# Kernel optimization log

Hardware: AMD Instinct MI355X
Metric: run time of the kernel (lower is better)

## Reference

```python
import jax, jax.numpy as jnp
from jax import lax
import numpy as np

TAU = 2.0      # LIF membrane time constant
VTH = 1.0      # spikingjelly LIFNode default v_threshold
ALPHA = 2.0    # spikingjelly surrogate.ATan default alpha

# Heaviside spike with ATan surrogate gradient (spikingjelly semantics)
@jax.custom_vjp
def spike(x):
    return (x >= 0.0).astype(x.dtype)

def _spike_fwd(x):
    return spike(x), x

def _spike_bwd(x, g):
    sg = (ALPHA / 2.0) / (1.0 + (jnp.pi / 2.0 * ALPHA * x) ** 2)
    return (g * sg,)

spike.defvjp(_spike_fwd, _spike_bwd)

def lif_step(v, x):
    # decay_input=True, v_reset=0.0, hard reset (spikingjelly LIFNode defaults)
    v = v + (x - v) / TAU
    s = spike(v - VTH)
    v = v * (1.0 - s)
    return v, s

def conv1d_same(x, k):
    # x: [N, L], k: [K]  -> depthwise-style 1D conv with SAME padding
    y = lax.conv_general_dilated(x[:, None, :], k[None, None, :], (1,), 'SAME')
    return y[:, 0, :]

def setup_inputs() -> dict:
    key = jax.random.key(0)
    ks = jax.random.split(key, 16)
    N, T, D, C, NC = 4096, 16, 700, 128, 20
    def lin(kw, kb, fout, fin):
        s = 1.0 / np.sqrt(fin)
        W = jax.random.uniform(kw, (fout, fin), jnp.float32, -s, s)
        b = jax.random.uniform(kb, (fout,), jnp.float32, -s, s)
        return W, b
    x = jax.random.normal(ks[0], (N, T, D), jnp.float32)
    W_in, b_in = lin(ks[1], ks[2], C, D)
    W_rec, b_rec = lin(ks[3], ks[4], C, C)
    W2, b2 = lin(ks[5], ks[6], C, C)
    k_t = jax.random.normal(ks[7], (3,), jnp.float32) * 0.5   # TATCA temporal conv, kernel_size_t=3
    k_c = jax.random.normal(ks[8], (3,), jnp.float32) * 0.5   # TATCA channel conv
    W_p, b_p = lin(ks[9], ks[10], C, C)
    W_out, b_out = lin(ks[11], ks[12], NC, C)
    return {"x": x, "W_in": W_in, "b_in": b_in, "W_rec": W_rec, "b_rec": b_rec,
            "W2": W2, "b2": b2, "k_t": k_t, "k_c": k_c,
            "W_p": W_p, "b_p": b_p, "W_out": W_out, "b_out": b_out}

def reference(x, W_in, b_in, W_rec, b_rec, W2, b2, k_t, k_c, W_p, b_p, W_out, b_out):
    N, T, D = x.shape
    C = W_in.shape[0]
    z = jnp.zeros((N, C), x.dtype)

    def step(carry, frame):
        v1, v2, spikes_last = carry
        inp = frame @ W_in.T + b_in + spikes_last @ W_rec.T + b_rec
        v1, s1 = lif_step(v1, inp)
        x2 = s1 @ W2.T + b2
        v2, feat = lif_step(v2, x2)
        return (v1, v2, s1), feat

    xs = jnp.transpose(x, (1, 0, 2))          # [T, N, D]
    _, features = lax.scan(step, (z, z, z), xs)  # [T, N, C]

    # TATCA_1D: temporal attention (conv over T, kernel 3) x channel attention (conv over C)
    t_att = jax.nn.sigmoid(conv1d_same(features.mean(2).T, k_t)).T   # [T, N]
    c_att = jax.nn.sigmoid(conv1d_same(features.mean(0), k_c))       # [N, C]
    attended = features * t_att[:, :, None] * c_att[None, :, :]

    def step2(v3, feat):
        h = feat @ W_p.T + b_p
        v3, s = lif_step(v3, h)
        return v3, s @ W_out.T + b_out

    _, outs = lax.scan(step2, z, attended)    # [T, N, num_classes]
    return outs.mean(0), features, attended
```

## Files before the change

kernel.cpp:

```cpp
#include <hip/hip_runtime.h>
#include <hip/hip_bf16.h>
#include <stdint.h>


typedef __attribute__((ext_vector_type(8))) _Float16 half8;
typedef __attribute__((ext_vector_type(4))) float f32x4;
typedef unsigned long long u64;

#define MFMA16F(a, b, c) __builtin_amdgcn_mfma_f32_16x16x32_f16(a, b, c, 0, 0, 0)

__device__ inline void gload16(const void* g, void* l) {
  __builtin_amdgcn_global_load_lds(
      (const __attribute__((address_space(1))) uint32_t*)g,
      (__attribute__((address_space(3))) uint32_t*)l, 16, 0, 0);
}

__device__ inline void splitf16(float4 q0, float4 q1, half8& hh, half8& ll) {
  float f[8] = {q0.x, q0.y, q0.z, q0.w, q1.x, q1.y, q1.z, q1.w};
  _Float16 H[8], L[8];
#pragma unroll
  for (int j = 0; j < 8; ++j) {
    _Float16 h1 = (_Float16)(f[j] * 16.0f);
    float r = fmaf((float)h1, -0.0625f, f[j]);
    L[j] = (_Float16)(r * 32768.0f);
    H[j] = h1;
  }
  __builtin_memcpy(&hh, H, 16);
  __builtin_memcpy(&ll, L, 16);
}

__global__ void k_prep(const float* __restrict__ Wr, const float* __restrict__ W2,
                       const float* __restrict__ Wp, const float* __restrict__ Win,
                       float* __restrict__ WrT, float* __restrict__ W2T,
                       float* __restrict__ WpT, ushort* __restrict__ F2) {
  int idx = blockIdx.x * blockDim.x + threadIdx.x;
  if (idx < 3 * 16384) {
    int sel = idx >> 14;
    int r = idx & 16383;
    int j = r >> 7, c = r & 127;
    const float* src = (sel == 0) ? Wr : (sel == 1) ? W2 : Wp;
    float* dst = (sel == 0) ? WrT : (sel == 1) ? W2T : WpT;
    dst[r] = src[c * 128 + j];
  } else {
    int i2 = idx - 49152;
    if (i2 >= 128 * 704) return;
    int c = i2 / 704, d = i2 - c * 704;
    float w = (d < 700) ? Win[c * 700 + d] : 0.f;
    _Float16 b1 = (_Float16)(w * 256.0f);
    float r = fmaf((float)b1, -0.00390625f, w);
    _Float16 b2 = (_Float16)(r * 524288.0f);
    ushort u1, u2;
    __builtin_memcpy(&u1, &b1, 2);
    __builtin_memcpy(&u2, &b2, 2);
    F2[i2] = u1;
    F2[90112 + i2] = u2;
  }
}

__global__ __launch_bounds__(256, 4) void k_gemm_scan(
    const float* __restrict__ x, const ushort* __restrict__ F2,
    const float* __restrict__ b_in, const float* __restrict__ b_rec,
    const float* __restrict__ WrT, const float* __restrict__ W2T,
    const float* __restrict__ b2, const float* __restrict__ WpT,
    const float* __restrict__ b_p, const float* __restrict__ W_out,
    const float* __restrict__ b_out, const float* __restrict__ k_t,
    const float* __restrict__ k_c, float* __restrict__ features,
    float* __restrict__ attended, float* __restrict__ out0) {
  __shared__ __align__(16) char lds[39424];

  const int tid = threadIdx.x;
  const int w = tid >> 6;
  const int l = tid & 63;
  const int blk = blockIdx.x;
  const int lm = l & 15, kh = l >> 4;

  const float* xr = x + (size_t)(blk * 64 + w * 16 + lm) * 700;

  const ushort* bsrc[4];
  int bdst[4];
#pragma unroll
  for (int i = 0; i < 4; ++i) {
    int idx = w * 4 + i;
    int plane = idx >> 3, cg = idx & 7;
    int col = cg * 16 + (l >> 2);
    bsrc[i] = F2 + plane * 90112 + col * 704 + (((l & 3) ^ ((l >> 3) & 3)) * 8);
    bdst[i] = plane * 8192 + cg * 1024;
  }
  const int bkey = (lm >> 1) & 3;
  const int brd = lm * 64 + ((kh ^ bkey) * 16);

  f32x4 acc_h[8], acc_m[8];
#pragma unroll
  for (int j = 0; j < 8; ++j) {
    acc_h[j] = (f32x4){0.f, 0.f, 0.f, 0.f};
    acc_m[j] = (f32x4){0.f, 0.f, 0.f, 0.f};
  }

  auto STAGE = [&](int buf, int kt) {
    const int k0 = kt * 32;
#pragma unroll
    for (int i = 0; i < 4; ++i)
      gload16(bsrc[i] + k0, lds + buf * 16384 + bdst[i]);
  };
  auto LOADA = [&](int kt, float4& q0, float4& q1) {
    const int k0 = kt * 32 + kh * 8;
    q0 = *(const float4*)(xr + k0);
    if (kt == 21 && kh == 3)
      q1 = make_float4(0.f, 0.f, 0.f, 0.f);
    else
      q1 = *(const float4*)(xr + k0 + 4);
  };

  STAGE(0, 0);
  float4 qa, qb;
  LOADA(0, qa, qb);
  __syncthreads();
  int buf = 0;
  for (int kt = 0; kt < 22; ++kt) {
    float4 na = {}, nb = {};
    if (kt < 21) {
      STAGE(buf ^ 1, kt + 1);
      LOADA(kt + 1, na, nb);
    }
    half8 a1, a2;
    splitf16(qa, qb, a1, a2);
    const char* bb0 = lds + buf * 16384 + brd;
#pragma unroll
    for (int nf = 0; nf < 8; ++nf) {
      const char* bb = bb0 + nf * 1024;
      half8 b1 = *(const half8*)(bb);
      half8 b2f = *(const half8*)(bb + 8192);
      acc_h[nf] = MFMA16F(a1, b1, acc_h[nf]);
      acc_m[nf] = MFMA16F(a1, b2f, acc_m[nf]);
      acc_m[nf] = MFMA16F(a2, b1, acc_m[nf]);
    }
    __syncthreads();
    qa = na; qb = nb;
    buf ^= 1;
  }

  float* XWs = (float*)lds;
#pragma unroll
  for (int nf = 0; nf < 8; ++nf) {
    const int col = nf * 16 + lm;
    const float bias = b_in[col] + b_rec[col];
    const int rowb = w * 16 + kh * 4;
#pragma unroll
    for (int r = 0; r < 4; ++r)
      XWs[(rowb + r) * 130 + col] =
          acc_h[nf][r] * 0.000244140625f +
          acc_m[nf][r] * 1.1920928955078125e-7f + bias;
  }

  const int n_glob = blk * 4 + w;
  char* sc = lds + 33280 + w * 1536;
  u64* fmaskp = (u64*)sc;
  float* tap = (float*)(sc + 256);
  float* cap = (float*)(sc + 320);
  float* gp = (float*)(sc + 832);

  const float b2a = b2[l], b2b = b2[l + 64];
  float v1a = 0.f, v1b = 0.f, v2a = 0.f, v2b = 0.f, fsa = 0.f, fsb = 0.f;
  u64 pm0 = 0ull, pm1 = 0ull;

  for (int t = 0; t < 16; ++t) {
    const float* xrow = XWs + (w * 16 + t) * 130;
    float ia = xrow[l];
    float ib = xrow[l + 64];
    u64 q0 = pm0, q1 = pm1;
    while (q0) { int j = __builtin_ctzll(q0); q0 &= q0 - 1;
      ia += WrT[j * 128 + l]; ib += WrT[j * 128 + l + 64]; }
    while (q1) { int j = __builtin_ctzll(q1); q1 &= q1 - 1;
      ia += WrT[(64 + j) * 128 + l]; ib += WrT[(64 + j) * 128 + l + 64]; }
    v1a = v1a + (ia - v1a) * 0.5f;
    bool sa = (v1a - 1.0f) >= 0.f; v1a = sa ? 0.f : v1a;
    v1b = v1b + (ib - v1b) * 0.5f;
    bool sb = (v1b - 1.0f) >= 0.f; v1b = sb ? 0.f : v1b;
    pm0 = __ballot((int)sa);
    pm1 = __ballot((int)sb);
    float xa = b2a, xb = b2b;
    u64 r0 = pm0, r1 = pm1;
    while (r0) { int j = __builtin_ctzll(r0); r0 &= r0 - 1;
      xa += W2T[j * 128 + l]; xb += W2T[j * 128 + l + 64]; }
    while (r1) { int j = __builtin_ctzll(r1); r1 &= r1 - 1;
      xa += W2T[(64 + j) * 128 + l]; xb += W2T[(64 + j) * 128 + l + 64]; }
    v2a = v2a + (xa - v2a) * 0.5f;
    bool fa = (v2a - 1.0f) >= 0.f; v2a = fa ? 0.f : v2a;
    v2b = v2b + (xb - v2b) * 0.5f;
    bool fb = (v2b - 1.0f) >= 0.f; v2b = fb ? 0.f : v2b;
    float ffa = fa ? 1.f : 0.f, ffb = fb ? 1.f : 0.f;
    features[(size_t)((t << 12) | n_glob) * 128 + l] = ffa;
    features[(size_t)((t << 12) | n_glob) * 128 + l + 64] = ffb;
    fsa += ffa; fsb += ffb;
    u64 f0 = __ballot((int)fa), f1 = __ballot((int)fb);
    if (l == 0) { fmaskp[t * 2 + 0] = f0; fmaskp[t * 2 + 1] = f1; }
  }

  gp[l] = fsa * (1.f / 16.f);
  gp[l + 64] = fsb * (1.f / 16.f);

  if (l < 16) {
    float acc = 0.f;
#pragma unroll
    for (int j = 0; j < 3; ++j) {
      int tt = l - 1 + j;
      if (tt >= 0 && tt < 16) {
        float m = (float)(__popcll(fmaskp[tt * 2 + 0]) +
                          __popcll(fmaskp[tt * 2 + 1])) * (1.f / 128.f);
        acc += k_t[j] * m;
      }
    }
    tap[l] = 1.f / (1.f + expf(-acc));
  }
  {
    float mm1 = (l == 0) ? 0.f : gp[l - 1];
    float acc = k_c[0] * mm1 + k_c[1] * gp[l] + k_c[2] * gp[l + 1];
    cap[l] = 1.f / (1.f + expf(-acc));
    float np1 = (l == 63) ? 0.f : gp[l + 65];
    float acc2 = k_c[0] * gp[l + 63] + k_c[1] * gp[l + 64] + k_c[2] * np1;
    cap[l + 64] = 1.f / (1.f + expf(-acc2));
  }

  const float bpa = b_p[l], bpb = b_p[l + 64];
  const float caa = cap[l], cab = cap[l + 64];
  float v3a = 0.f, v3b = 0.f, ssa = 0.f, ssb = 0.f;
  for (int t = 0; t < 16; ++t) {
    u64 m0 = fmaskp[t * 2 + 0], m1 = fmaskp[t * 2 + 1];
    float tat = tap[t];
    bool ba = (m0 >> l) & 1, bb = (m1 >> l) & 1;
    attended[(size_t)((t << 12) | n_glob) * 128 + l] = ba ? tat * caa : 0.f;
    attended[(size_t)((t << 12) | n_glob) * 128 + l + 64] = bb ? tat * cab : 0.f;
    float ha = bpa, hb = bpb;
    u64 q0 = m0, q1 = m1;
    while (q0) { int j = __builtin_ctzll(q0); q0 &= q0 - 1;
      float w_ = tat * cap[j];
      ha += w_ * WpT[j * 128 + l]; hb += w_ * WpT[j * 128 + l + 64]; }
    while (q1) { int j = __builtin_ctzll(q1); q1 &= q1 - 1;
      float w_ = tat * cap[64 + j];
      ha += w_ * WpT[(64 + j) * 128 + l]; hb += w_ * WpT[(64 + j) * 128 + l + 64]; }
    v3a = v3a + (ha - v3a) * 0.5f;
    bool sa = (v3a - 1.0f) >= 0.f; v3a = sa ? 0.f : v3a;
    ssa += sa ? 1.f : 0.f;
    v3b = v3b + (hb - v3b) * 0.5f;
    bool sb = (v3b - 1.0f) >= 0.f; v3b = sb ? 0.f : v3b;
    ssb += sb ? 1.f : 0.f;
  }
  gp[l] = ssa * (1.f / 16.f);
  gp[l + 64] = ssb * (1.f / 16.f);
  if (l < 20) {
    float acc = b_out[l];
    for (int j = 0; j < 128; ++j) acc += gp[j] * W_out[l * 128 + j];
    out0[n_glob * 20 + l] = acc;
  }
}

extern "C" void kernel_launch(void* const* d_in, const int* in_sizes, int n_in,
                              void* d_out, int out_size, void* d_ws, size_t ws_size,
                              hipStream_t stream) {
  const float* x     = (const float*)d_in[0];
  const float* W_in  = (const float*)d_in[1];
  const float* b_in  = (const float*)d_in[2];
  const float* W_rec = (const float*)d_in[3];
  const float* b_rec = (const float*)d_in[4];
  const float* W2    = (const float*)d_in[5];
  const float* b2    = (const float*)d_in[6];
  const float* k_t   = (const float*)d_in[7];
  const float* k_c   = (const float*)d_in[8];
  const float* W_p   = (const float*)d_in[9];
  const float* b_p   = (const float*)d_in[10];
  const float* W_out = (const float*)d_in[11];
  const float* b_out = (const float*)d_in[12];

  float* out      = (float*)d_out;
  float* out0     = out;
  float* features = out + 81920;
  float* attended = out + 81920 + 8388608;

  float* ws  = (float*)d_ws;
  float* WrT = ws;
  float* W2T = ws + 16384;
  float* WpT = ws + 32768;
  ushort* F2 = (ushort*)(ws + 49152);

  hipLaunchKernelGGL(k_prep, dim3(544), dim3(256), 0, stream,
                     W_rec, W2, W_p, W_in, WrT, W2T, WpT, F2);
  hipLaunchKernelGGL(k_gemm_scan, dim3(1024), dim3(256), 0, stream,
                     x, F2, b_in, b_rec, WrT, W2T, b2, WpT, b_p, W_out, b_out,
                     k_t, k_c, features, attended, out0);
}
```

Measured before the change: 74.69 us.

## Deepen A-operand prefetch to two stages with explicit vmcnt waits and priority

Register prefetch of the x input tiles now runs two iterations ahead instead of one, and the generic __syncthreads is replaced by raw s_barrier calls guarded by sched_barriers and a manual s_waitcnt vmcnt(6). This is meant to hide global-load latency of the fp32 input stream behind MFMA work. It also raises wave priority around the MFMA block. The cost is more live registers, plus a correctness risk: the hand-coded vmcnt count must match the number of outstanding loads.

```diff
diff --git a/kernel.cpp b/kernel.cpp
--- a/kernel.cpp
+++ b/kernel.cpp
@@ -112,19 +112,28 @@
   };
 
   STAGE(0, 0);
-  float4 qa, qb;
-  LOADA(0, qa, qb);
+  float4 qa0, qb0, qa1, qb1;
+  LOADA(0, qa0, qb0);
+  LOADA(1, qa1, qb1);
   __syncthreads();
+
   int buf = 0;
   for (int kt = 0; kt < 22; ++kt) {
-    float4 na = {}, nb = {};
-    if (kt < 21) {
-      STAGE(buf ^ 1, kt + 1);
-      LOADA(kt + 1, na, nb);
-    }
+    if (kt < 21) STAGE(buf ^ 1, kt + 1);
+    float4 na = make_float4(0.f, 0.f, 0.f, 0.f);
+    float4 nb = make_float4(0.f, 0.f, 0.f, 0.f);
+    if (kt < 20) LOADA(kt + 2, na, nb);
+    __builtin_amdgcn_sched_barrier(0);
+    if (kt < 21) asm volatile("s_waitcnt vmcnt(6)" ::: "memory");
+    else         asm volatile("s_waitcnt vmcnt(0)" ::: "memory");
+    __builtin_amdgcn_sched_barrier(0);
+    __builtin_amdgcn_s_barrier();
+    __builtin_amdgcn_sched_barrier(0);
+
     half8 a1, a2;
-    splitf16(qa, qb, a1, a2);
+    splitf16(qa0, qb0, a1, a2);
     const char* bb0 = lds + buf * 16384 + brd;
+    __builtin_amdgcn_s_setprio(1);
 #pragma unroll
     for (int nf = 0; nf < 8; ++nf) {
       const char* bb = bb0 + nf * 1024;
@@ -134,8 +143,11 @@
       acc_m[nf] = MFMA16F(a1, b2f, acc_m[nf]);
       acc_m[nf] = MFMA16F(a2, b1, acc_m[nf]);
     }
-    __syncthreads();
-    qa = na; qb = nb;
+    __builtin_amdgcn_s_setprio(0);
+    __builtin_amdgcn_sched_barrier(0);
+    __builtin_amdgcn_s_barrier();
+    __builtin_amdgcn_sched_barrier(0);
+    qa0 = qa1; qb0 = qb1; qa1 = na; qb1 = nb;
     buf ^= 1;
   }
 
```

Result: slower. 88.27 us (+18.2%).

## Replace LDS scratch with wave shuffles, swizzle XW tile, raise occupancy

Applied to the files above, without the earlier changes.

Removes the per-wave LDS scratch for spike masks, attention vectors and means, keeping them in registers and reading them with cross-lane shuffles. The padded 130-stride XW tile becomes a 128-stride tile with an XOR swizzle to avoid bank conflicts. Shared memory drops from 39424 to 32768 bytes and launch bounds go from 4 to 5 blocks per SM for more occupancy. Shuffles inside the sparse spike loops add per-iteration cross-lane work, and the tighter register budget may cause spills.

```diff
diff --git a/kernel.cpp b/kernel.cpp
--- a/kernel.cpp
+++ b/kernel.cpp
@@ -13,6 +13,12 @@
   __builtin_amdgcn_global_load_lds(
       (const __attribute__((address_space(1))) uint32_t*)g,
       (__attribute__((address_space(3))) uint32_t*)l, 16, 0, 0);
+}
+
+__device__ inline u64 shfl64(u64 v, int src) {
+  int lo = __shfl((int)(unsigned)(v & 0xffffffffu), src);
+  int hi = __shfl((int)(unsigned)(v >> 32), src);
+  return ((u64)(unsigned)hi << 32) | (unsigned)lo;
 }
 
 __device__ inline void splitf16(float4 q0, float4 q1, half8& hh, half8& ll) {
@@ -57,7 +63,7 @@
   }
 }
 
-__global__ __launch_bounds__(256, 4) void k_gemm_scan(
+__global__ __launch_bounds__(256, 5) void k_gemm_scan(
     const float* __restrict__ x, const ushort* __restrict__ F2,
     const float* __restrict__ b_in, const float* __restrict__ b_rec,
     const float* __restrict__ WrT, const float* __restrict__ W2T,
@@ -66,7 +72,7 @@
     const float* __restrict__ b_out, const float* __restrict__ k_t,
     const float* __restrict__ k_c, float* __restrict__ features,
     float* __restrict__ attended, float* __restrict__ out0) {
-  __shared__ __align__(16) char lds[39424];
+  __shared__ __align__(16) char lds[32768];
 
   const int tid = threadIdx.x;
   const int w = tid >> 6;
@@ -144,29 +150,28 @@
   for (int nf = 0; nf < 8; ++nf) {
     const int col = nf * 16 + lm;
     const float bias = b_in[col] + b_rec[col];
+    const int colx = col ^ (kh << 3);
     const int rowb = w * 16 + kh * 4;
 #pragma unroll
     for (int r = 0; r < 4; ++r)
-      XWs[(rowb + r) * 130 + col] =
+      XWs[(rowb + r) * 128 + colx] =
           acc_h[nf][r] * 0.000244140625f +
           acc_m[nf][r] * 1.1920928955078125e-7f + bias;
   }
 
   const int n_glob = blk * 4 + w;
-  char* sc = lds + 33280 + w * 1536;
-  u64* fmaskp = (u64*)sc;
-  float* tap = (float*)(sc + 256);
-  float* cap = (float*)(sc + 320);
-  float* gp = (float*)(sc + 832);
 
   const float b2a = b2[l], b2b = b2[l + 64];
   float v1a = 0.f, v1b = 0.f, v2a = 0.f, v2b = 0.f, fsa = 0.f, fsb = 0.f;
   u64 pm0 = 0ull, pm1 = 0ull;
+  u64 fm0 = 0ull, fm1 = 0ull;
+  float pcv = 0.f;
 
   for (int t = 0; t < 16; ++t) {
-    const float* xrow = XWs + (w * 16 + t) * 130;
-    float ia = xrow[l];
-    float ib = xrow[l + 64];
+    const float* xrow = XWs + (w * 16 + t) * 128;
+    const int key = ((t >> 2) & 3) << 3;
+    float ia = xrow[l ^ key];
+    float ib = xrow[(l + 64) ^ key];
     u64 q0 = pm0, q1 = pm1;
     while (q0) { int j = __builtin_ctzll(q0); q0 &= q0 - 1;
       ia += WrT[j * 128 + l]; ib += WrT[j * 128 + l + 64]; }
@@ -193,50 +198,56 @@
     features[(size_t)((t << 12) | n_glob) * 128 + l + 64] = ffb;
     fsa += ffa; fsb += ffb;
     u64 f0 = __ballot((int)fa), f1 = __ballot((int)fb);
-    if (l == 0) { fmaskp[t * 2 + 0] = f0; fmaskp[t * 2 + 1] = f1; }
-  }
-
-  gp[l] = fsa * (1.f / 16.f);
-  gp[l + 64] = fsb * (1.f / 16.f);
-
-  if (l < 16) {
+    if (l == t) {
+      fm0 = f0; fm1 = f1;
+      pcv = (float)(__popcll(f0) + __popcll(f1));
+    }
+  }
+
+  const float msa = fsa * (1.f / 16.f);
+  const float msb = fsb * (1.f / 16.f);
+
+  float tav = 0.f;
+  {
     float acc = 0.f;
 #pragma unroll
     for (int j = 0; j < 3; ++j) {
       int tt = l - 1 + j;
+      float pv = __shfl(pcv, (tt & 63));
       if (tt >= 0 && tt < 16) {
-        float m = (float)(__popcll(fmaskp[tt * 2 + 0]) +
-                          __popcll(fmaskp[tt * 2 + 1])) * (1.f / 128.f);
+        float m = pv * (1.f / 128.f);
         acc += k_t[j] * m;
       }
     }
-    tap[l] = 1.f / (1.f + expf(-acc));
-  }
+    tav = 1.f / (1.f + expf(-acc));
+  }
+  float caa, cab;
   {
-    float mm1 = (l == 0) ? 0.f : gp[l - 1];
-    float acc = k_c[0] * mm1 + k_c[1] * gp[l] + k_c[2] * gp[l + 1];
-    cap[l] = 1.f / (1.f + expf(-acc));
-    float np1 = (l == 63) ? 0.f : gp[l + 65];
-    float acc2 = k_c[0] * gp[l + 63] + k_c[1] * gp[l + 64] + k_c[2] * np1;
-    cap[l + 64] = 1.f / (1.f + expf(-acc2));
+    float lft = __shfl(msa, (l == 0) ? 0 : (l - 1));
+    float nm1 = (l == 0) ? 0.f : lft;
+    float rgt = (l == 63) ? __shfl(msb, 0) : __shfl(msa, (l + 1) & 63);
+    caa = 1.f / (1.f + expf(-(k_c[0] * nm1 + k_c[1] * msa + k_c[2] * rgt)));
+    float lftb = (l == 0) ? __shfl(msa, 63) : __shfl(msb, (l - 1) & 63);
+    float rgtb_raw = __shfl(msb, (l + 1) & 63);
+    float rgtb = (l == 63) ? 0.f : rgtb_raw;
+    cab = 1.f / (1.f + expf(-(k_c[0] * lftb + k_c[1] * msb + k_c[2] * rgtb)));
   }
 
   const float bpa = b_p[l], bpb = b_p[l + 64];
-  const float caa = cap[l], cab = cap[l + 64];
   float v3a = 0.f, v3b = 0.f, ssa = 0.f, ssb = 0.f;
   for (int t = 0; t < 16; ++t) {
-    u64 m0 = fmaskp[t * 2 + 0], m1 = fmaskp[t * 2 + 1];
-    float tat = tap[t];
+    u64 m0 = shfl64(fm0, t), m1 = shfl64(fm1, t);
+    float tat = __shfl(tav, t);
     bool ba = (m0 >> l) & 1, bb = (m1 >> l) & 1;
     attended[(size_t)((t << 12) | n_glob) * 128 + l] = ba ? tat * caa : 0.f;
     attended[(size_t)((t << 12) | n_glob) * 128 + l + 64] = bb ? tat * cab : 0.f;
     float ha = bpa, hb = bpb;
     u64 q0 = m0, q1 = m1;
     while (q0) { int j = __builtin_ctzll(q0); q0 &= q0 - 1;
-      float w_ = tat * cap[j];
+      float w_ = tat * __shfl(caa, j);
       ha += w_ * WpT[j * 128 + l]; hb += w_ * WpT[j * 128 + l + 64]; }
     while (q1) { int j = __builtin_ctzll(q1); q1 &= q1 - 1;
-      float w_ = tat * cap[64 + j];
+      float w_ = tat * __shfl(cab, j);
       ha += w_ * WpT[(64 + j) * 128 + l]; hb += w_ * WpT[(64 + j) * 128 + l + 64]; }
     v3a = v3a + (ha - v3a) * 0.5f;
     bool sa = (v3a - 1.0f) >= 0.f; v3a = sa ? 0.f : v3a;
@@ -245,12 +256,15 @@
     bool sb = (v3b - 1.0f) >= 0.f; v3b = sb ? 0.f : v3b;
     ssb += sb ? 1.f : 0.f;
   }
-  gp[l] = ssa * (1.f / 16.f);
-  gp[l + 64] = ssb * (1.f / 16.f);
-  if (l < 20) {
-    float acc = b_out[l];
-    for (int j = 0; j < 128; ++j) acc += gp[j] * W_out[l * 128 + j];
-    out0[n_glob * 20 + l] = acc;
+  const float gsa = ssa * (1.f / 16.f);
+  const float gsb = ssb * (1.f / 16.f);
+
+  {
+    const float* wrow = W_out + (size_t)((l < 20) ? l : 0) * 128;
+    float acc = (l < 20) ? b_out[l] : 0.f;
+    for (int j = 0; j < 64; ++j) acc += __shfl(gsa, j) * wrow[j];
+    for (int j = 0; j < 64; ++j) acc += __shfl(gsb, j) * wrow[64 + j];
+    if (l < 20) out0[n_glob * 20 + l] = acc;
   }
 }
 
```

New measurement: 125.4 us. 1.68x slower.
